# Optimization experiments

Hardware: AMD Instinct MI355X
Metric: run time of the kernel (lower is better)

Reference implementation:

```python
import jax, jax.numpy as jnp
import numpy as np

N = 4096   # number of nodes
E = 4096   # number of hyperedges
F_IN = 128
F_OUT = 128
AVG_DEG = 32.0


def setup_inputs() -> dict:
    key = jax.random.key(0)
    k_x, k_h, k_w = jax.random.split(key, 3)
    X = jax.random.normal(k_x, (N, F_IN), dtype=jnp.float32)
    # Binary incidence matrix with average node degree ~AVG_DEG
    H = (jax.random.uniform(k_h, (N, E)) < (AVG_DEG / E)).astype(jnp.float32)
    # Diagonal degree matrices (clamped >= 1 so they are invertible)
    dv = jnp.maximum(H.sum(axis=1), 1.0)   # [N] vertex degrees
    de = jnp.maximum(H.sum(axis=0), 1.0)   # [E] hyperedge degrees
    D_v = jnp.diag(dv)                     # [N, N]
    D_e = jnp.diag(de)                     # [E, E]
    # Xavier-uniform weight
    limit = float(np.sqrt(6.0 / (F_IN + F_OUT)))
    W = jax.random.uniform(k_w, (F_IN, F_OUT), minval=-limit, maxval=limit,
                           dtype=jnp.float32)
    return {"X": X, "H": H, "D_v": D_v, "D_e": D_e, "W": W}


def reference(X, H, D_v, D_e, W):
    # Faithful to torch: generic matrix inverse of the (diagonal) degree matrices
    D_v_inv = jnp.linalg.inv(D_v)          # [N, N]
    D_e_inv = jnp.linalg.inv(D_e)          # [E, E]
    theta = X @ W                          # [N, F_out]
    coeff = D_v_inv @ H                    # [N, E]
    coeff = coeff @ D_e_inv                # [N, E]
    coeff = coeff @ H.T                    # [N, N]
    return coeff @ theta                   # [N, F_out]
```

## Files before the change

### kernel.cpp

```cpp
#include <hip/hip_runtime.h>

constexpr int N = 4096;
constexpr int E = 4096;
constexpr int F = 128;
constexpr int MAXL = 128;
constexpr int DIAG_LD = 4097;

__device__ __forceinline__ ushort f2bf_rne(float x) {
    union { float f; unsigned u; } v; v.f = x;
    return (ushort)((v.u + 0x7FFFu + ((v.u >> 16) & 1u)) >> 16);
}

__global__ __launch_bounds__(256) void k_theta(const float* __restrict__ X,
                                               const float* __restrict__ W,
                                               ushort* __restrict__ theta_bf) {
    __shared__ float Xs[16][F];
    const int t = threadIdx.x;
    const int r0 = blockIdx.x * 16;
    #pragma unroll
    for (int i = 0; i < 2; ++i) {
        const int idx = i * 256 + t;
        const int rr = idx >> 5, cc = (idx & 31) * 4;
        *(float4*)&Xs[rr][cc] = *(const float4*)&X[(size_t)(r0 + rr) * F + cc];
    }
    __syncthreads();
    const int f = t & 127, half = t >> 7;
    float acc[8];
    #pragma unroll
    for (int i = 0; i < 8; ++i) acc[i] = 0.f;
    #pragma unroll 4
    for (int k = 0; k < F; ++k) {
        const float w = W[k * F + f];
        #pragma unroll
        for (int i = 0; i < 8; ++i) acc[i] += Xs[half * 8 + i][k] * w;
    }
    #pragma unroll
    for (int i = 0; i < 8; ++i)
        theta_bf[(size_t)(r0 + half * 8 + i) * F + f] = f2bf_rne(acc[i]);
}

__global__ __launch_bounds__(256) void k_pass1(const float* __restrict__ H,
                                               unsigned long long* __restrict__ BM,
                                               int* __restrict__ row_cnt,
                                               ushort* __restrict__ row_list) {
    __shared__ ushort sL[4][MAXL];
    __shared__ int lcnt[4];
    const int t = threadIdx.x, wave = t >> 6, lane = t & 63;
    if (lane == 0) lcnt[wave] = 0;
    const int r = blockIdx.x * 4 + wave;
    const float* Hr = H + (size_t)r * E;
    #pragma unroll
    for (int half = 0; half < 2; ++half) {
        uint4 v[8];
        #pragma unroll
        for (int q = 0; q < 8; ++q)
            v[q] = *(const uint4*)&Hr[((half * 8 + q) * 64 + lane) * 4];
        unsigned long long wreg = 0;
        #pragma unroll
        for (int q = 0; q < 8; ++q) {
            const int i = half * 8 + q;
            const uint vv[4] = {v[q].x, v[q].y, v[q].z, v[q].w};
            #pragma unroll
            for (int c = 0; c < 4; ++c) {
                const unsigned long long m = __ballot(vv[c] != 0u);
                const int widx = q * 4 + c;
                if (lane == widx) wreg = m;
                if (vv[c]) {
                    const int p = atomicAdd(&lcnt[wave], 1);
                    if (p < MAXL) sL[wave][p] = (ushort)(i * 256 + 4 * lane + c);
                }
            }
        }
        if (lane < 32)
            BM[(size_t)r * 64 + half * 32 + lane] = wreg;
    }
    const int cnt = lcnt[wave] < MAXL ? lcnt[wave] : MAXL;
    ((uint*)&row_list[(size_t)r * MAXL])[lane] = ((const uint*)sL[wave])[lane];
    if (lane == 0) row_cnt[r] = cnt;
}

__global__ __launch_bounds__(512) void k_pass2(
        const unsigned long long* __restrict__ BM,
        int* __restrict__ col_cnt,
        ushort* __restrict__ col_list) {
    __shared__ ushort sL[64][MAXL];
    __shared__ int cnt[64];
    const int t = threadIdx.x, wave = t >> 6, lane = t & 63;
    const int wc = blockIdx.x;
    if (t < 64) cnt[t] = 0;
    __syncthreads();
    unsigned long long w8[8];
    #pragma unroll
    for (int j = 0; j < 8; ++j)
        w8[j] = BM[(size_t)(wave * 512 + j * 64 + lane) * 64 + wc];
    #pragma unroll
    for (int j = 0; j < 8; ++j) {
        unsigned long long m = w8[j];
        const ushort row = (ushort)(wave * 512 + j * 64 + lane);
        while (m) {
            const int b = __builtin_ctzll(m); m &= m - 1;
            const int p = atomicAdd(&cnt[b], 1);
            if (p < MAXL) sL[b][p] = row;
        }
    }
    __syncthreads();
    const int el = t >> 3, ch = t & 7;
    const int e = (wc >> 2) * 256 + 4 * el + (wc & 3);
    const uint4* src = (const uint4*)sL[el];
    uint4* dst = (uint4*)&col_list[(size_t)e * MAXL];
    dst[ch * 2 + 0] = src[ch * 2 + 0];
    dst[ch * 2 + 1] = src[ch * 2 + 1];
    if (ch == 0) col_cnt[e] = cnt[el] < MAXL ? cnt[el] : MAXL;
}

template <bool OUT_BF16>
__global__ __launch_bounds__(256) void k_spmm(const int* __restrict__ cnt,
                                              const ushort* __restrict__ list,
                                              const ushort* __restrict__ Vin,
                                              const float* __restrict__ Dmat,
                                              void* __restrict__ Vout) {
    __shared__ ushort sIdx[4][MAXL];
    const int t = threadIdx.x, wave = t >> 6, lane = t & 63;
    const int r = blockIdx.x * 4 + wave;
    *(ushort2*)&sIdx[wave][lane * 2] =
        *(const ushort2*)&list[(size_t)r * MAXL + lane * 2];
    int c = cnt[r]; c = c < MAXL ? c : MAXL;
    const float dscale = 1.0f / Dmat[(size_t)r * DIAG_LD];
    __syncthreads();
    const char* vb = (const char*)Vin;
    float a0 = 0.f, a1 = 0.f;
    int i = 0;
    for (; i + 8 <= c; i += 8) {
        uint v[8];
        #pragma unroll
        for (int j = 0; j < 8; ++j)
            v[j] = *(const uint*)(vb + ((int)sIdx[wave][i + j] * 256 + lane * 4));
        #pragma unroll
        for (int j = 0; j < 8; ++j) {
            a0 += __uint_as_float((v[j] & 0xffffu) << 16);
            a1 += __uint_as_float((v[j] >> 16) << 16);
        }
    }
    for (; i < c; ++i) {
        const uint v = *(const uint*)(vb + ((int)sIdx[wave][i] * 256 + lane * 4));
        a0 += __uint_as_float((v & 0xffffu) << 16);
        a1 += __uint_as_float((v >> 16) << 16);
    }
    a0 *= dscale; a1 *= dscale;
    if (OUT_BF16) {
        ushort2 o; o.x = f2bf_rne(a0); o.y = f2bf_rne(a1);
        *(ushort2*)((ushort*)Vout + (size_t)r * F + lane * 2) = o;
    } else {
        float2 o; o.x = a0; o.y = a1;
        *(float2*)((float*)Vout + (size_t)r * F + lane * 2) = o;
    }
}

extern "C" void kernel_launch(void* const* d_in, const int* in_sizes, int n_in,
                              void* d_out, int out_size, void* d_ws, size_t ws_size,
                              hipStream_t stream) {
    const float* X  = (const float*)d_in[0];
    const float* H  = (const float*)d_in[1];
    const float* Dv = (const float*)d_in[2];
    const float* De = (const float*)d_in[3];
    const float* W  = (const float*)d_in[4];
    float* out = (float*)d_out;
    char* ws = (char*)d_ws;

    ushort* theta    = (ushort*)ws;
    unsigned long long* BM =
        (unsigned long long*)(ws + (size_t)1 * 1024 * 1024);
    ushort* M        = (ushort*)(ws + (size_t)1 * 1024 * 1024);
    ushort* row_list = (ushort*)(ws + (size_t)3 * 1024 * 1024);
    ushort* col_list = (ushort*)(ws + (size_t)4 * 1024 * 1024);
    int*    row_cnt  = (int*)   (ws + (size_t)5 * 1024 * 1024);
    int*    col_cnt  = row_cnt + N;

    k_theta<<<dim3(N / 16), dim3(256), 0, stream>>>(X, W, theta);
    k_pass1<<<dim3(N / 4), dim3(256), 0, stream>>>(H, BM, row_cnt, row_list);
    k_pass2<<<dim3(64), dim3(512), 0, stream>>>(BM, col_cnt, col_list);
    k_spmm<true ><<<dim3(E / 4), dim3(256), 0, stream>>>(col_cnt, col_list,
                                                         theta, De, M);
    k_spmm<false><<<dim3(N / 4), dim3(256), 0, stream>>>(row_cnt, row_list,
                                                         M, Dv, out);
}
```

Baseline: 207.1 us.

## Fuse theta GEMM into H scan kernel, one row per block, deeper gather unroll

Merges the X@W theta kernel and the H incidence scan into a single launch, with extra blocks past N handling theta so the two independent jobs overlap and one launch is saved. The H scan now assigns one row per 256-thread block instead of one row per wave, adding a block-level barrier and a shared counter. The SpMM gather loop is unrolled to 16 loads with a 4-wide tail so more loads are in flight. The fused kernel's shared memory is sized for the larger theta branch, which may limit how many scan blocks fit per CU.

```diff
diff --git a/kernel.cpp b/kernel.cpp
--- a/kernel.cpp
+++ b/kernel.cpp
@@ -11,72 +11,75 @@
     return (ushort)((v.u + 0x7FFFu + ((v.u >> 16) & 1u)) >> 16);
 }
 
-__global__ __launch_bounds__(256) void k_theta(const float* __restrict__ X,
-                                               const float* __restrict__ W,
-                                               ushort* __restrict__ theta_bf) {
-    __shared__ float Xs[16][F];
+__global__ __launch_bounds__(256) void k_fused1(
+        const float* __restrict__ H,
+        const float* __restrict__ X,
+        const float* __restrict__ Wm,
+        unsigned long long* __restrict__ BM,
+        int* __restrict__ row_cnt,
+        ushort* __restrict__ row_list,
+        ushort* __restrict__ theta_bf) {
+    __shared__ float smem[16 * F];
     const int t = threadIdx.x;
-    const int r0 = blockIdx.x * 16;
-    #pragma unroll
-    for (int i = 0; i < 2; ++i) {
-        const int idx = i * 256 + t;
-        const int rr = idx >> 5, cc = (idx & 31) * 4;
-        *(float4*)&Xs[rr][cc] = *(const float4*)&X[(size_t)(r0 + rr) * F + cc];
-    }
-    __syncthreads();
-    const int f = t & 127, half = t >> 7;
-    float acc[8];
-    #pragma unroll
-    for (int i = 0; i < 8; ++i) acc[i] = 0.f;
-    #pragma unroll 4
-    for (int k = 0; k < F; ++k) {
-        const float w = W[k * F + f];
-        #pragma unroll
-        for (int i = 0; i < 8; ++i) acc[i] += Xs[half * 8 + i][k] * w;
-    }
-    #pragma unroll
-    for (int i = 0; i < 8; ++i)
-        theta_bf[(size_t)(r0 + half * 8 + i) * F + f] = f2bf_rne(acc[i]);
-}
-
-__global__ __launch_bounds__(256) void k_pass1(const float* __restrict__ H,
-                                               unsigned long long* __restrict__ BM,
-                                               int* __restrict__ row_cnt,
-                                               ushort* __restrict__ row_list) {
-    __shared__ ushort sL[4][MAXL];
-    __shared__ int lcnt[4];
-    const int t = threadIdx.x, wave = t >> 6, lane = t & 63;
-    if (lane == 0) lcnt[wave] = 0;
-    const int r = blockIdx.x * 4 + wave;
-    const float* Hr = H + (size_t)r * E;
-    #pragma unroll
-    for (int half = 0; half < 2; ++half) {
-        uint4 v[8];
-        #pragma unroll
-        for (int q = 0; q < 8; ++q)
-            v[q] = *(const uint4*)&Hr[((half * 8 + q) * 64 + lane) * 4];
+
+    if (blockIdx.x < (unsigned)N) {
+        ushort* sL   = (ushort*)smem;
+        int*    lcnt = (int*)(smem + 128);
+        const int wave = t >> 6, lane = t & 63;
+        if (t == 0) *lcnt = 0;
+        __syncthreads();
+        const int r = blockIdx.x;
+        const float* Hr = H + (size_t)r * E;
+        uint4 v[4];
+        #pragma unroll
+        for (int s = 0; s < 4; ++s)
+            v[s] = *(const uint4*)&Hr[(wave * 256 + s * 64 + lane) * 4];
         unsigned long long wreg = 0;
         #pragma unroll
-        for (int q = 0; q < 8; ++q) {
-            const int i = half * 8 + q;
-            const uint vv[4] = {v[q].x, v[q].y, v[q].z, v[q].w};
+        for (int s = 0; s < 4; ++s) {
+            const uint vv[4] = {v[s].x, v[s].y, v[s].z, v[s].w};
             #pragma unroll
             for (int c = 0; c < 4; ++c) {
                 const unsigned long long m = __ballot(vv[c] != 0u);
-                const int widx = q * 4 + c;
-                if (lane == widx) wreg = m;
+                if (lane == s * 4 + c) wreg = m;
                 if (vv[c]) {
-                    const int p = atomicAdd(&lcnt[wave], 1);
-                    if (p < MAXL) sL[wave][p] = (ushort)(i * 256 + 4 * lane + c);
+                    const int p = atomicAdd(lcnt, 1);
+                    if (p < MAXL)
+                        sL[p] = (ushort)(wave * 1024 + s * 256 + 4 * lane + c);
                 }
             }
         }
-        if (lane < 32)
-            BM[(size_t)r * 64 + half * 32 + lane] = wreg;
-    }
-    const int cnt = lcnt[wave] < MAXL ? lcnt[wave] : MAXL;
-    ((uint*)&row_list[(size_t)r * MAXL])[lane] = ((const uint*)sL[wave])[lane];
-    if (lane == 0) row_cnt[r] = cnt;
+        if (lane < 16)
+            BM[(size_t)r * 64 + wave * 16 + lane] = wreg;
+        __syncthreads();
+        if (wave == 0) {
+            ((uint*)&row_list[(size_t)r * MAXL])[lane] = ((const uint*)sL)[lane];
+            if (lane == 0) row_cnt[r] = *lcnt < MAXL ? *lcnt : MAXL;
+        }
+    } else {
+        float (*Xs)[F] = (float(*)[F])smem;
+        const int r0 = (blockIdx.x - N) * 16;
+        #pragma unroll
+        for (int i = 0; i < 2; ++i) {
+            const int idx = i * 256 + t;
+            const int rr = idx >> 5, cc = (idx & 31) * 4;
+            *(float4*)&Xs[rr][cc] = *(const float4*)&X[(size_t)(r0 + rr) * F + cc];
+        }
+        __syncthreads();
+        const int f = t & 127, half = t >> 7;
+        float acc[8];
+        #pragma unroll
+        for (int i = 0; i < 8; ++i) acc[i] = 0.f;
+        #pragma unroll 4
+        for (int k = 0; k < F; ++k) {
+            const float w = Wm[k * F + f];
+            #pragma unroll
+            for (int i = 0; i < 8; ++i) acc[i] += Xs[half * 8 + i][k] * w;
+        }
+        #pragma unroll
+        for (int i = 0; i < 8; ++i)
+            theta_bf[(size_t)(r0 + half * 8 + i) * F + f] = f2bf_rne(acc[i]);
+    }
 }
 
 __global__ __launch_bounds__(512) void k_pass2(
@@ -130,13 +133,24 @@
     const char* vb = (const char*)Vin;
     float a0 = 0.f, a1 = 0.f;
     int i = 0;
-    for (; i + 8 <= c; i += 8) {
-        uint v[8];
-        #pragma unroll
-        for (int j = 0; j < 8; ++j)
+    for (; i + 16 <= c; i += 16) {
+        uint v[16];
+        #pragma unroll
+        for (int j = 0; j < 16; ++j)
             v[j] = *(const uint*)(vb + ((int)sIdx[wave][i + j] * 256 + lane * 4));
         #pragma unroll
-        for (int j = 0; j < 8; ++j) {
+        for (int j = 0; j < 16; ++j) {
+            a0 += __uint_as_float((v[j] & 0xffffu) << 16);
+            a1 += __uint_as_float((v[j] >> 16) << 16);
+        }
+    }
+    for (; i + 4 <= c; i += 4) {
+        uint v[4];
+        #pragma unroll
+        for (int j = 0; j < 4; ++j)
+            v[j] = *(const uint*)(vb + ((int)sIdx[wave][i + j] * 256 + lane * 4));
+        #pragma unroll
+        for (int j = 0; j < 4; ++j) {
             a0 += __uint_as_float((v[j] & 0xffffu) << 16);
             a1 += __uint_as_float((v[j] >> 16) << 16);
         }
@@ -176,8 +190,8 @@
     int*    row_cnt  = (int*)   (ws + (size_t)5 * 1024 * 1024);
     int*    col_cnt  = row_cnt + N;
 
-    k_theta<<<dim3(N / 16), dim3(256), 0, stream>>>(X, W, theta);
-    k_pass1<<<dim3(N / 4), dim3(256), 0, stream>>>(H, BM, row_cnt, row_list);
+    k_fused1<<<dim3(N + N / 16), dim3(256), 0, stream>>>(
+        H, X, W, BM, row_cnt, row_list, theta);
     k_pass2<<<dim3(64), dim3(512), 0, stream>>>(BM, col_cnt, col_list);
     k_spmm<true ><<<dim3(E / 4), dim3(256), 0, stream>>>(col_cnt, col_list,
                                                          theta, De, M);
```

Result: faster. 199.4 us (-3.7%).
